# Kernel optimization log

Measured on AMD Instinct MI355X. Metric: run time of the kernel, lower is better.

Reference implementation:

```python
import jax, jax.numpy as jnp
import numpy as np
from jax import lax

GAMMA = 0.001  # init kwarg gamma
DN = ('NCHW', 'OIHW', 'NCHW')


def _maxpool2(x):
    # 2x2 max pool, stride 2, NCHW
    return lax.reduce_window(x, -jnp.inf, lax.max, (1, 1, 2, 2), (1, 1, 2, 2), 'VALID')


def _features(x, w1, b1, w2, b2):
    h = lax.conv_general_dilated(x, w1, (1, 1), 'SAME', dimension_numbers=DN)
    h = _maxpool2(jax.nn.relu(h + b1[None, :, None, None]))
    h = lax.conv_general_dilated(h, w2, (1, 1), 'SAME', dimension_numbers=DN)
    h = _maxpool2(jax.nn.relu(h + b2[None, :, None, None]))
    return h.reshape(h.shape[0], -1)  # [N, 16*7*7=784]


def setup_inputs() -> dict:
    key = jax.random.key(0)
    ks = jax.random.split(key, 7)
    x = jax.random.normal(ks[0], (4096, 1, 28, 28), dtype=jnp.float32)
    w1 = jax.random.normal(ks[1], (8, 1, 3, 3), dtype=jnp.float32) * 0.1
    b1 = jax.random.normal(ks[2], (8,), dtype=jnp.float32) * 0.1
    w2 = jax.random.normal(ks[3], (16, 8, 3, 3), dtype=jnp.float32) * 0.1
    b2 = jax.random.normal(ks[4], (16,), dtype=jnp.float32) * 0.1
    support = jax.random.uniform(ks[5], (8192, 784), dtype=jnp.float32)
    alpha = jax.random.normal(ks[6], (8192, 4), dtype=jnp.float32)
    return {'x': x, 'w1': w1, 'b1': b1, 'w2': w2, 'b2': b2,
            'support': support, 'alpha': alpha}


def reference(x, w1, b1, w2, b2, support, alpha):
    feats = _features(x, w1, b1, w2, b2)                      # [N, 784]
    # Pairwise squared distances via expansion (replaces the N*M python loop)
    f2 = jnp.sum(feats * feats, axis=1, keepdims=True)        # [N, 1]
    s2 = jnp.sum(support * support, axis=1)[None, :]          # [1, M]
    d2 = f2 + s2 - 2.0 * (feats @ support.T)                  # [N, M]
    K = jnp.exp(-GAMMA * d2)                                  # RBF kernel matrix
    return K @ alpha                                          # [N, n_classes]
```

## Files before the change

kernel.cpp:

```cpp
#include <hip/hip_runtime.h>
#include <hip/hip_bf16.h>
#include <cstdint>

#define GAMMA 0.001f
#define TILE_BYTES 114688

typedef __attribute__((ext_vector_type(4))) float f32x4;
typedef __attribute__((ext_vector_type(8))) int v8i;
typedef __attribute__((ext_vector_type(8))) short bh8;
typedef unsigned char u8;

__device__ inline unsigned pack4_fp8(float4 f) {
  unsigned p = __builtin_amdgcn_cvt_pk_fp8_f32(f.x, f.y, 0, false);
  p = __builtin_amdgcn_cvt_pk_fp8_f32(f.z, f.w, p, true);
  return p;
}

__device__ inline ushort bf16u(float v) {
  __hip_bfloat16 h = __float2bfloat16(v);
  return *(ushort*)&h;
}

__global__ __launch_bounds__(256, 4) void conv_prep_kernel(
    const float* __restrict__ x, const float* __restrict__ w1,
    const float* __restrict__ b1, const float* __restrict__ w2,
    const float* __restrict__ b2, const float* __restrict__ support,
    const float* __restrict__ alpha, u8* __restrict__ feats_t,
    u8* __restrict__ sup_t, float* __restrict__ beta,
    float* __restrict__ ef) {
  int tid = threadIdx.x;
  int bx = blockIdx.x;

  if (bx >= 2048) {
    int lane = tid & 63, wave = tid >> 6;
    int m = (bx - 2048) * 4 + wave;
    const float* row = support + (size_t)m * 784;
    int mt = m >> 7, mr = m & 127;
    u8* tb = sup_t + (size_t)mt * TILE_BYTES;
    float ss = 0.f;
    if (lane < 56) {
      uint4 w;
      if (lane < 49) {
        float4 f0 = ((const float4*)row)[lane * 4 + 0];
        float4 f1 = ((const float4*)row)[lane * 4 + 1];
        float4 f2 = ((const float4*)row)[lane * 4 + 2];
        float4 f3 = ((const float4*)row)[lane * 4 + 3];
        ss = f0.x * f0.x + f0.y * f0.y + f0.z * f0.z + f0.w * f0.w +
             f1.x * f1.x + f1.y * f1.y + f1.z * f1.z + f1.w * f1.w +
             f2.x * f2.x + f2.y * f2.y + f2.z * f2.z + f2.w * f2.w +
             f3.x * f3.x + f3.y * f3.y + f3.z * f3.z + f3.w * f3.w;
        w.x = pack4_fp8(f0); w.y = pack4_fp8(f1);
        w.z = pack4_fp8(f2); w.w = pack4_fp8(f3);
      } else {
        w.x = 0; w.y = 0; w.z = 0; w.w = 0;
      }
      int kk = lane >> 3, u = lane & 7, q = u >> 1, h = u & 1;
      int qs = q ^ ((mr >> 1) & 3);
      *(uint4*)(tb + kk * 16384 + h * 8192 + mr * 64 + qs * 16) = w;
    }
#pragma unroll
    for (int s = 1; s < 64; s <<= 1) ss += __shfl_xor(ss, s, 64);
    if (lane == 0) {
      float es = __expf(-GAMMA * ss);
      float4 a = ((const float4*)alpha)[m];
      float4 b;
      b.x = es * a.x; b.y = es * a.y; b.z = es * a.z; b.w = es * a.w;
      ((float4*)beta)[m] = b;
    }
    return;
  }

  __shared__ float xp[2][900];
  __shared__ alignas(16) ushort a1h[2][2048];
  __shared__ float w1s[72], b1s[8], b2s[16];
  __shared__ float w2s[1152];
  __shared__ alignas(8) ushort sc[2][16][212];
  __shared__ alignas(16) u8 fb[2][784];
  __shared__ float red[256];

  int lane = tid & 63, wave = tid >> 6;

  for (int t = tid; t < 1800; t += 256) ((float*)xp)[t] = 0.f;
  for (int t = tid; t < 1024; t += 256) ((uint4*)a1h)[t] = (uint4){0, 0, 0, 0};
  if (tid < 72) w1s[tid] = w1[tid];
  if (tid < 8) b1s[tid] = b1[tid];
  if (tid < 16) b2s[tid] = b2[tid];
  for (int t = tid; t < 1152; t += 256) w2s[t] = w2[t];
  __syncthreads();

  int oc = lane & 15, quad = lane >> 4;
  bh8 wf[3];
#pragma unroll
  for (int g = 0; g < 3; g++) {
    int tap = g * 4 + quad;
#pragma unroll
    for (int j = 0; j < 8; j++) {
      float v = (tap < 9) ? w2s[oc * 72 + j * 9 + tap] : 0.f;
      wf[g][j] = (short)bf16u(v);
    }
  }

  for (int t = tid; t < 392; t += 256) {
    int img = t >= 196, j = t - img * 196;
    float4 v = ((const float4*)(x + (size_t)(bx * 2 + img) * 784))[j];
    int r = j / 7, c = (j % 7) * 4;
    float* p = &xp[img][(r + 1) * 30 + (c + 1)];
    p[0] = v.x; p[1] = v.y; p[2] = v.z; p[3] = v.w;
  }
  __syncthreads();

  for (int idx = tid; idx < 3136; idx += 256) {
    int img = idx >= 1568;
    int rem = idx - img * 1568;
    int c = rem / 196, r2 = rem % 196;
    int ph = r2 / 14, pw = r2 % 14;
    const float* w = &w1s[c * 9];
    const float* xb = &xp[img][(2 * ph) * 30 + (2 * pw)];
    float t[4][4];
#pragma unroll
    for (int a = 0; a < 4; a++) {
      float2 u0 = *(const float2*)(xb + a * 30);
      float2 u1 = *(const float2*)(xb + a * 30 + 2);
      t[a][0] = u0.x; t[a][1] = u0.y; t[a][2] = u1.x; t[a][3] = u1.y;
    }
    float s00 = 0, s01 = 0, s10 = 0, s11 = 0;
#pragma unroll
    for (int dy = 0; dy < 3; dy++)
#pragma unroll
      for (int dx = 0; dx < 3; dx++) {
        float wv = w[dy * 3 + dx];
        s00 += t[dy][dx] * wv;     s01 += t[dy][dx + 1] * wv;
        s10 += t[dy + 1][dx] * wv; s11 += t[dy + 1][dx + 1] * wv;
      }
    float mx = fmaxf(fmaxf(s00, s01), fmaxf(s10, s11));
    float val = fmaxf(mx + b1s[c], 0.f);
    a1h[img][((ph + 1) * 16 + (pw + 1)) * 8 + c] = bf16u(val);
  }
  __syncthreads();

  {
    int img2 = wave >> 1, half = wave & 1;
    int Tstart = half * 7, Tcnt = half ? 6 : 7;
    const ushort* abase = a1h[img2];
    int mrow = lane & 15;
    for (int t = 0; t < Tcnt; ++t) {
      int T = Tstart + t;
      int p = T * 16 + mrow;
      int pc = p > 195 ? 195 : p;
      int y = pc / 14, xq = pc - y * 14;
      int cell = y * 16 + xq;
      f32x4 acc = (f32x4){0, 0, 0, 0};
#pragma unroll
      for (int g = 0; g < 3; g++) {
        int tap = g * 4 + quad;
        const ushort* ap;
        if (g == 2 && quad > 0) {
          ap = abase;
        } else {
          int dy = tap / 3, dx = tap - dy * 3;
          ap = abase + (cell + dy * 16 + dx) * 8;
        }
        bh8 af = *(const bh8*)ap;
        acc = __builtin_amdgcn_mfma_f32_16x16x32_bf16(af, wf[g], acc, 0, 0, 0);
      }
      int pos0 = T * 16 + quad * 4;
      ushort4 s4;
      s4.x = bf16u(acc.x); s4.y = bf16u(acc.y);
      s4.z = bf16u(acc.z); s4.w = bf16u(acc.w);
      *(ushort4*)(&sc[img2][oc][pos0]) = s4;
    }
  }
  __syncthreads();

  int img = tid >> 7, r = tid & 127;
  float fsq = 0.f;
  if (r < 112) {
    int o = r & 15, y7 = r >> 4;
    const ushort* srow = sc[img][o];
    float bo = b2s[o];
#pragma unroll
    for (int x7 = 0; x7 < 7; x7++) {
      int p = 28 * y7 + 2 * x7;
      unsigned u0 = *(const unsigned*)(&srow[p]);
      unsigned u1 = *(const unsigned*)(&srow[p + 14]);
      float a = __uint_as_float(u0 << 16);
      float b = __uint_as_float(u0 & 0xffff0000u);
      float c = __uint_as_float(u1 << 16);
      float d = __uint_as_float(u1 & 0xffff0000u);
      float mx = fmaxf(fmaxf(a, b), fmaxf(c, d));
      float val = fmaxf(mx + bo, 0.f);
      fb[img][o * 49 + y7 * 7 + x7] =
          (u8)(__builtin_amdgcn_cvt_pk_fp8_f32(val, 0.f, 0, false) & 0xff);
      fsq += val * val;
    }
  }
  red[tid] = fsq;
  __syncthreads();
  for (int s = 64; s > 0; s >>= 1) {
    if ((tid & 127) < s) red[tid] += red[tid + s];
    __syncthreads();
  }
  if ((tid & 127) == 0) ef[bx * 2 + img] = __expf(-GAMMA * red[tid]);

  if (tid < 112) {
    int im = tid >= 56, j = tid - im * 56;
    uint4 v;
    if (j < 49) v = ((const uint4*)fb[im])[j];
    else { v.x = 0; v.y = 0; v.z = 0; v.w = 0; }
    int n = bx * 2 + im;
    int nt = n >> 7, nr = n & 127;
    int kk = j >> 3, u = j & 7, q = u >> 1, h = u & 1;
    int qs = q ^ ((nr >> 1) & 3);
    *(uint4*)(feats_t + (size_t)nt * TILE_BYTES + kk * 16384 + h * 8192 +
              nr * 64 + qs * 16) = v;
  }
}

__global__ __launch_bounds__(256, 4) void rbf_gemm_kernel(
    const u8* __restrict__ feats_t, const u8* __restrict__ sup_t,
    const float* __restrict__ beta, float* __restrict__ partial) {
  int tid = threadIdx.x;
  int wave = tid >> 6, lane = tid & 63;
  int bx = blockIdx.x;
  int chunk = bx & 63, nb = bx >> 6;
  int wn = wave >> 1, wm = wave & 1;
  int col = lane & 15, quad = lane >> 4;
  int slot = quad ^ ((col >> 1) & 3);

  const u8* abase = feats_t + (size_t)nb * TILE_BYTES +
                    (wn * 64 + col) * 64 + slot * 16;
  const u8* bbase = sup_t + (size_t)chunk * TILE_BYTES +
                    (wm * 64 + col) * 64 + slot * 16;

  f32x4 acc[4][4];
#pragma unroll
  for (int i = 0; i < 4; i++)
#pragma unroll
    for (int j = 0; j < 4; j++) acc[i][j] = (f32x4){0, 0, 0, 0};

#define LDFRAG(p)                                                      \
  ({                                                                   \
    int4 lo_ = *(const int4*)(p);                                      \
    int4 hi_ = *(const int4*)((p) + 8192);                             \
    (v8i){lo_.x, lo_.y, lo_.z, lo_.w, hi_.x, hi_.y, hi_.z, hi_.w};     \
  })
#define MFMA(a, b, c)                                                  \
  __builtin_amdgcn_mfma_scale_f32_16x16x128_f8f6f4(                    \
      (a), (b), (c), 0, 0, 0, 0x7f7f7f7f, 0, 0x7f7f7f7f)

#pragma unroll 1
  for (int kk = 0; kk < 7; ++kk) {
    const u8* ak = abase + kk * 16384;
    const u8* bk = bbase + kk * 16384;
    v8i bv0 = LDFRAG(bk);
    v8i bv1 = LDFRAG(bk + 1024);
    v8i bv2 = LDFRAG(bk + 2048);
    v8i bv3 = LDFRAG(bk + 3072);
    v8i a0 = LDFRAG(ak);
    v8i a1 = LDFRAG(ak + 1024);
    acc[0][0] = MFMA(a0, bv0, acc[0][0]);
    acc[0][1] = MFMA(a0, bv1, acc[0][1]);
    acc[0][2] = MFMA(a0, bv2, acc[0][2]);
    acc[0][3] = MFMA(a0, bv3, acc[0][3]);
    a0 = LDFRAG(ak + 2048);
    acc[1][0] = MFMA(a1, bv0, acc[1][0]);
    acc[1][1] = MFMA(a1, bv1, acc[1][1]);
    acc[1][2] = MFMA(a1, bv2, acc[1][2]);
    acc[1][3] = MFMA(a1, bv3, acc[1][3]);
    a1 = LDFRAG(ak + 3072);
    acc[2][0] = MFMA(a0, bv0, acc[2][0]);
    acc[2][1] = MFMA(a0, bv1, acc[2][1]);
    acc[2][2] = MFMA(a0, bv2, acc[2][2]);
    acc[2][3] = MFMA(a0, bv3, acc[2][3]);
    acc[3][0] = MFMA(a1, bv0, acc[3][0]);
    acc[3][1] = MFMA(a1, bv1, acc[3][1]);
    acc[3][2] = MFMA(a1, bv2, acc[3][2]);
    acc[3][3] = MFMA(a1, bv3, acc[3][3]);
  }
#undef LDFRAG
#undef MFMA

#pragma unroll
  for (int i = 0; i < 4; i++)
#pragma unroll
    for (int j = 0; j < 4; j++) {
      acc[i][j].x = __expf(2.f * GAMMA * acc[i][j].x);
      acc[i][j].y = __expf(2.f * GAMMA * acc[i][j].y);
      acc[i][j].z = __expf(2.f * GAMMA * acc[i][j].z);
      acc[i][j].w = __expf(2.f * GAMMA * acc[i][j].w);
    }
  int n0 = nb * 128, m0 = chunk * 128;
#pragma unroll
  for (int c = 0; c < 4; ++c) {
    float bl[4];
#pragma unroll
    for (int j = 0; j < 4; j++)
      bl[j] = beta[(m0 + wm * 64 + j * 16 + col) * 4 + c];
#pragma unroll
    for (int i = 0; i < 4; i++) {
      f32x4 s = acc[i][0] * bl[0] + acc[i][1] * bl[1] + acc[i][2] * bl[2] +
                acc[i][3] * bl[3];
#pragma unroll
      for (int st = 1; st < 16; st <<= 1) {
        s.x += __shfl_xor(s.x, st, 16);
        s.y += __shfl_xor(s.y, st, 16);
        s.z += __shfl_xor(s.z, st, 16);
        s.w += __shfl_xor(s.w, st, 16);
      }
      if (col == c) {
        int n = n0 + wn * 64 + i * 16 + quad * 4;
        float* pp = partial + (((size_t)chunk * 2 + wm) * 4096 + n) * 4 + c;
        pp[0] = s.x; pp[4] = s.y; pp[8] = s.z; pp[12] = s.w;
      }
    }
  }
}

__global__ __launch_bounds__(256) void reduce_kernel(
    const float* __restrict__ partial, const float* __restrict__ ef,
    float* __restrict__ out) {
  __shared__ float4 sred[16][16];
  int nl = threadIdx.x & 15, sg = threadIdx.x >> 4;
  int n = blockIdx.x * 16 + nl;
  const float4* p = (const float4*)partial;
  float sx = 0, sy = 0, sz = 0, sw = 0;
#pragma unroll
  for (int ch = sg * 8; ch < sg * 8 + 8; ch++) {
    float4 v = p[(size_t)ch * 4096 + n];
    sx += v.x; sy += v.y; sz += v.z; sw += v.w;
  }
  sred[sg][nl] = (float4){sx, sy, sz, sw};
  __syncthreads();
  for (int st = 8; st > 0; st >>= 1) {
    if (sg < st) {
      float4 a = sred[sg][nl], b = sred[sg + st][nl];
      sred[sg][nl] = (float4){a.x + b.x, a.y + b.y, a.z + b.z, a.w + b.w};
    }
    __syncthreads();
  }
  if (sg == 0) {
    float e = ef[n];
    float4 a = sred[0][nl];
    ((float4*)out)[n] = (float4){e * a.x, e * a.y, e * a.z, e * a.w};
  }
}

extern "C" void kernel_launch(void* const* d_in, const int* in_sizes, int n_in,
                              void* d_out, int out_size, void* d_ws,
                              size_t ws_size, hipStream_t stream) {
  const float* x = (const float*)d_in[0];
  const float* w1 = (const float*)d_in[1];
  const float* b1 = (const float*)d_in[2];
  const float* w2 = (const float*)d_in[3];
  const float* b2 = (const float*)d_in[4];
  const float* support = (const float*)d_in[5];
  const float* alpha = (const float*)d_in[6];
  float* out = (float*)d_out;

  u8* ws = (u8*)d_ws;
  u8* sup_t = ws;
  u8* feats_t = ws + 7340032;
  float* beta = (float*)(ws + 11010048);
  float* ef = (float*)(ws + 11141120);
  float* partial = (float*)(ws + 11157504);

  conv_prep_kernel<<<4096, 256, 0, stream>>>(x, w1, b1, w2, b2, support, alpha,
                                             feats_t, sup_t, beta, ef);
  rbf_gemm_kernel<<<2048, 256, 0, stream>>>(feats_t, sup_t, beta, partial);
  reduce_kernel<<<256, 256, 0, stream>>>(partial, ef, out);
}
```

Before: 160.3 us.

## Fuse three kernels into one persistent cooperative kernel with grid syncs

Replaces the three separate launches (conv+prep, RBF GEMM, reduce) with a single cooperative persistent kernel. It loops over the original block indices and separates the phases with grid-wide syncs. The goal is to remove launch gaps and inter-kernel drain between phases. The costs are a smaller grid that may reduce occupancy for the heavy phases, two grid barriers, and extra shared-memory pressure from the fused kernel. If the cooperative launch fails, the code falls back to the original three launches.

```diff
diff --git a/kernel.cpp b/kernel.cpp
--- a/kernel.cpp
+++ b/kernel.cpp
@@ -1,6 +1,9 @@
 #include <hip/hip_runtime.h>
 #include <hip/hip_bf16.h>
+#include <hip/hip_cooperative_groups.h>
 #include <cstdint>
+
+namespace cg = cooperative_groups;
 
 #define GAMMA 0.001f
 #define TILE_BYTES 114688
@@ -19,6 +22,334 @@
 __device__ inline ushort bf16u(float v) {
   __hip_bfloat16 h = __float2bfloat16(v);
   return *(ushort*)&h;
+}
+
+__global__ __launch_bounds__(256, 4) void fused_kernel(
+    const float* __restrict__ x, const float* __restrict__ w1,
+    const float* __restrict__ b1, const float* __restrict__ w2,
+    const float* __restrict__ b2, const float* __restrict__ support,
+    const float* __restrict__ alpha, u8* __restrict__ feats_t,
+    u8* __restrict__ sup_t, float* __restrict__ beta, float* __restrict__ ef,
+    float* __restrict__ partial, float* __restrict__ out) {
+  __shared__ alignas(16) float xp[2][900];
+  __shared__ alignas(16) ushort a1h[2][2048];
+  __shared__ float w1s[72], b1s[8], b2s[16];
+  __shared__ float w2s[1152];
+  __shared__ alignas(8) ushort sc[2][16][212];
+  __shared__ alignas(16) u8 fb[2][784];
+  __shared__ float red[256];
+
+  int tid = threadIdx.x;
+  int lane = tid & 63, wave = tid >> 6;
+
+  for (int cbx = blockIdx.x; cbx < 2048; cbx += gridDim.x) {
+    __syncthreads();
+
+    for (int t = tid; t < 1800; t += 256) ((float*)xp)[t] = 0.f;
+    for (int t = tid; t < 1024; t += 256)
+      ((uint4*)a1h)[t] = (uint4){0, 0, 0, 0};
+    if (tid < 72) w1s[tid] = w1[tid];
+    if (tid < 8) b1s[tid] = b1[tid];
+    if (tid < 16) b2s[tid] = b2[tid];
+    for (int t = tid; t < 1152; t += 256) w2s[t] = w2[t];
+    __syncthreads();
+
+    int oc = lane & 15, quad = lane >> 4;
+    bh8 wf[3];
+#pragma unroll
+    for (int g = 0; g < 3; g++) {
+      int tap = g * 4 + quad;
+#pragma unroll
+      for (int j = 0; j < 8; j++) {
+        float v = (tap < 9) ? w2s[oc * 72 + j * 9 + tap] : 0.f;
+        wf[g][j] = (short)bf16u(v);
+      }
+    }
+
+    for (int t = tid; t < 392; t += 256) {
+      int img = t >= 196, j = t - img * 196;
+      float4 v = ((const float4*)(x + (size_t)(cbx * 2 + img) * 784))[j];
+      int r = j / 7, c = (j % 7) * 4;
+      float* p = &xp[img][(r + 1) * 30 + (c + 1)];
+      p[0] = v.x; p[1] = v.y; p[2] = v.z; p[3] = v.w;
+    }
+    __syncthreads();
+
+    for (int idx = tid; idx < 3136; idx += 256) {
+      int img = idx >= 1568;
+      int rem = idx - img * 1568;
+      int c = rem / 196, r2 = rem % 196;
+      int ph = r2 / 14, pw = r2 % 14;
+      const float* w = &w1s[c * 9];
+      const float* xb = &xp[img][(2 * ph) * 30 + (2 * pw)];
+      float t[4][4];
+#pragma unroll
+      for (int a = 0; a < 4; a++) {
+        float2 u0 = *(const float2*)(xb + a * 30);
+        float2 u1 = *(const float2*)(xb + a * 30 + 2);
+        t[a][0] = u0.x; t[a][1] = u0.y; t[a][2] = u1.x; t[a][3] = u1.y;
+      }
+      float s00 = 0, s01 = 0, s10 = 0, s11 = 0;
+#pragma unroll
+      for (int dy = 0; dy < 3; dy++)
+#pragma unroll
+        for (int dx = 0; dx < 3; dx++) {
+          float wv = w[dy * 3 + dx];
+          s00 += t[dy][dx] * wv;     s01 += t[dy][dx + 1] * wv;
+          s10 += t[dy + 1][dx] * wv; s11 += t[dy + 1][dx + 1] * wv;
+        }
+      float mx = fmaxf(fmaxf(s00, s01), fmaxf(s10, s11));
+      float val = fmaxf(mx + b1s[c], 0.f);
+      a1h[img][((ph + 1) * 16 + (pw + 1)) * 8 + c] = bf16u(val);
+    }
+    __syncthreads();
+
+    {
+      int img2 = wave >> 1, half = wave & 1;
+      int Tstart = half * 7, Tcnt = half ? 6 : 7;
+      const ushort* abase = a1h[img2];
+      int mrow = lane & 15;
+      for (int t = 0; t < Tcnt; ++t) {
+        int T = Tstart + t;
+        int p = T * 16 + mrow;
+        int pc = p > 195 ? 195 : p;
+        int y = pc / 14, xq = pc - y * 14;
+        int cell = y * 16 + xq;
+        f32x4 acc = (f32x4){0, 0, 0, 0};
+#pragma unroll
+        for (int g = 0; g < 3; g++) {
+          int tap = g * 4 + quad;
+          const ushort* ap;
+          if (g == 2 && quad > 0) {
+            ap = abase;
+          } else {
+            int dy = tap / 3, dx = tap - dy * 3;
+            ap = abase + (cell + dy * 16 + dx) * 8;
+          }
+          bh8 af = *(const bh8*)ap;
+          acc =
+              __builtin_amdgcn_mfma_f32_16x16x32_bf16(af, wf[g], acc, 0, 0, 0);
+        }
+        int pos0 = T * 16 + quad * 4;
+        ushort4 s4;
+        s4.x = bf16u(acc.x); s4.y = bf16u(acc.y);
+        s4.z = bf16u(acc.z); s4.w = bf16u(acc.w);
+        *(ushort4*)(&sc[img2][oc][pos0]) = s4;
+      }
+    }
+    __syncthreads();
+
+    int img = tid >> 7, r = tid & 127;
+    float fsq = 0.f;
+    if (r < 112) {
+      int o = r & 15, y7 = r >> 4;
+      const ushort* srow = sc[img][o];
+      float bo = b2s[o];
+#pragma unroll
+      for (int x7 = 0; x7 < 7; x7++) {
+        int p = 28 * y7 + 2 * x7;
+        unsigned u0 = *(const unsigned*)(&srow[p]);
+        unsigned u1 = *(const unsigned*)(&srow[p + 14]);
+        float a = __uint_as_float(u0 << 16);
+        float b = __uint_as_float(u0 & 0xffff0000u);
+        float c = __uint_as_float(u1 << 16);
+        float d = __uint_as_float(u1 & 0xffff0000u);
+        float mx = fmaxf(fmaxf(a, b), fmaxf(c, d));
+        float val = fmaxf(mx + bo, 0.f);
+        fb[img][o * 49 + y7 * 7 + x7] =
+            (u8)(__builtin_amdgcn_cvt_pk_fp8_f32(val, 0.f, 0, false) & 0xff);
+        fsq += val * val;
+      }
+    }
+    red[tid] = fsq;
+    __syncthreads();
+    for (int s = 64; s > 0; s >>= 1) {
+      if ((tid & 127) < s) red[tid] += red[tid + s];
+      __syncthreads();
+    }
+    if ((tid & 127) == 0) ef[cbx * 2 + img] = __expf(-GAMMA * red[tid]);
+
+    if (tid < 112) {
+      int im = tid >= 56, j = tid - im * 56;
+      uint4 v;
+      if (j < 49) v = ((const uint4*)fb[im])[j];
+      else { v.x = 0; v.y = 0; v.z = 0; v.w = 0; }
+      int n = cbx * 2 + im;
+      int nt = n >> 7, nr = n & 127;
+      int kk = j >> 3, u = j & 7, q = u >> 1, h = u & 1;
+      int qs = q ^ ((nr >> 1) & 3);
+      *(uint4*)(feats_t + (size_t)nt * TILE_BYTES + kk * 16384 + h * 8192 +
+                nr * 64 + qs * 16) = v;
+    }
+  }
+
+  for (int sb = blockIdx.x; sb < 2048; sb += gridDim.x) {
+    int m = sb * 4 + wave;
+    const float* row = support + (size_t)m * 784;
+    int mt = m >> 7, mr = m & 127;
+    u8* tb = sup_t + (size_t)mt * TILE_BYTES;
+    float ss = 0.f;
+    if (lane < 56) {
+      uint4 w;
+      if (lane < 49) {
+        float4 f0 = ((const float4*)row)[lane * 4 + 0];
+        float4 f1 = ((const float4*)row)[lane * 4 + 1];
+        float4 f2 = ((const float4*)row)[lane * 4 + 2];
+        float4 f3 = ((const float4*)row)[lane * 4 + 3];
+        ss = f0.x * f0.x + f0.y * f0.y + f0.z * f0.z + f0.w * f0.w +
+             f1.x * f1.x + f1.y * f1.y + f1.z * f1.z + f1.w * f1.w +
+             f2.x * f2.x + f2.y * f2.y + f2.z * f2.z + f2.w * f2.w +
+             f3.x * f3.x + f3.y * f3.y + f3.z * f3.z + f3.w * f3.w;
+        w.x = pack4_fp8(f0); w.y = pack4_fp8(f1);
+        w.z = pack4_fp8(f2); w.w = pack4_fp8(f3);
+      } else {
+        w.x = 0; w.y = 0; w.z = 0; w.w = 0;
+      }
+      int kk = lane >> 3, u = lane & 7, q = u >> 1, h = u & 1;
+      int qs = q ^ ((mr >> 1) & 3);
+      *(uint4*)(tb + kk * 16384 + h * 8192 + mr * 64 + qs * 16) = w;
+    }
+#pragma unroll
+    for (int s = 1; s < 64; s <<= 1) ss += __shfl_xor(ss, s, 64);
+    if (lane == 0) {
+      float es = __expf(-GAMMA * ss);
+      float4 a = ((const float4*)alpha)[m];
+      float4 b;
+      b.x = es * a.x; b.y = es * a.y; b.z = es * a.z; b.w = es * a.w;
+      ((float4*)beta)[m] = b;
+    }
+  }
+
+  __threadfence();
+  cg::this_grid().sync();
+
+#define LDFRAG(p)                                                      \
+  ({                                                                   \
+    int4 lo_ = *(const int4*)(p);                                      \
+    int4 hi_ = *(const int4*)((p) + 8192);                             \
+    (v8i){lo_.x, lo_.y, lo_.z, lo_.w, hi_.x, hi_.y, hi_.z, hi_.w};     \
+  })
+#define MFMA(a, b, c)                                                  \
+  __builtin_amdgcn_mfma_scale_f32_16x16x128_f8f6f4(                    \
+      (a), (b), (c), 0, 0, 0, 0x7f7f7f7f, 0, 0x7f7f7f7f)
+
+  for (int gbx = blockIdx.x; gbx < 2048; gbx += gridDim.x) {
+    int chunk = gbx & 63, nb = gbx >> 6;
+    int wn = wave >> 1, wm = wave & 1;
+    int col = lane & 15, quad = lane >> 4;
+    int slot = quad ^ ((col >> 1) & 3);
+
+    const u8* abase = feats_t + (size_t)nb * TILE_BYTES +
+                      (wn * 64 + col) * 64 + slot * 16;
+    const u8* bbase = sup_t + (size_t)chunk * TILE_BYTES +
+                      (wm * 64 + col) * 64 + slot * 16;
+
+    f32x4 acc[4][4];
+#pragma unroll
+    for (int i = 0; i < 4; i++)
+#pragma unroll
+      for (int j = 0; j < 4; j++) acc[i][j] = (f32x4){0, 0, 0, 0};
+
+#pragma unroll 1
+    for (int kk = 0; kk < 7; ++kk) {
+      const u8* ak = abase + kk * 16384;
+      const u8* bk = bbase + kk * 16384;
+      v8i bv0 = LDFRAG(bk);
+      v8i bv1 = LDFRAG(bk + 1024);
+      v8i bv2 = LDFRAG(bk + 2048);
+      v8i bv3 = LDFRAG(bk + 3072);
+      v8i a0 = LDFRAG(ak);
+      v8i a1 = LDFRAG(ak + 1024);
+      acc[0][0] = MFMA(a0, bv0, acc[0][0]);
+      acc[0][1] = MFMA(a0, bv1, acc[0][1]);
+      acc[0][2] = MFMA(a0, bv2, acc[0][2]);
+      acc[0][3] = MFMA(a0, bv3, acc[0][3]);
+      a0 = LDFRAG(ak + 2048);
+      acc[1][0] = MFMA(a1, bv0, acc[1][0]);
+      acc[1][1] = MFMA(a1, bv1, acc[1][1]);
+      acc[1][2] = MFMA(a1, bv2, acc[1][2]);
+      acc[1][3] = MFMA(a1, bv3, acc[1][3]);
+      a1 = LDFRAG(ak + 3072);
+      acc[2][0] = MFMA(a0, bv0, acc[2][0]);
+      acc[2][1] = MFMA(a0, bv1, acc[2][1]);
+      acc[2][2] = MFMA(a0, bv2, acc[2][2]);
+      acc[2][3] = MFMA(a0, bv3, acc[2][3]);
+      acc[3][0] = MFMA(a1, bv0, acc[3][0]);
+      acc[3][1] = MFMA(a1, bv1, acc[3][1]);
+      acc[3][2] = MFMA(a1, bv2, acc[3][2]);
+      acc[3][3] = MFMA(a1, bv3, acc[3][3]);
+    }
+
+#pragma unroll
+    for (int i = 0; i < 4; i++)
+#pragma unroll
+      for (int j = 0; j < 4; j++) {
+        acc[i][j].x = __expf(2.f * GAMMA * acc[i][j].x);
+        acc[i][j].y = __expf(2.f * GAMMA * acc[i][j].y);
+        acc[i][j].z = __expf(2.f * GAMMA * acc[i][j].z);
+        acc[i][j].w = __expf(2.f * GAMMA * acc[i][j].w);
+      }
+    int n0 = nb * 128, m0 = chunk * 128;
+#pragma unroll
+    for (int c = 0; c < 4; ++c) {
+      float bl[4];
+#pragma unroll
+      for (int j = 0; j < 4; j++)
+        bl[j] = beta[(m0 + wm * 64 + j * 16 + col) * 4 + c];
+#pragma unroll
+      for (int i = 0; i < 4; i++) {
+        f32x4 s = acc[i][0] * bl[0] + acc[i][1] * bl[1] + acc[i][2] * bl[2] +
+                  acc[i][3] * bl[3];
+#pragma unroll
+        for (int st = 1; st < 16; st <<= 1) {
+          s.x += __shfl_xor(s.x, st, 16);
+          s.y += __shfl_xor(s.y, st, 16);
+          s.z += __shfl_xor(s.z, st, 16);
+          s.w += __shfl_xor(s.w, st, 16);
+        }
+        if (col == c) {
+          int n = n0 + wn * 64 + i * 16 + quad * 4;
+          float* pp = partial + (((size_t)chunk * 2 + wm) * 4096 + n) * 4 + c;
+          pp[0] = s.x; pp[4] = s.y; pp[8] = s.z; pp[12] = s.w;
+        }
+      }
+    }
+  }
+#undef LDFRAG
+#undef MFMA
+
+  __threadfence();
+  cg::this_grid().sync();
+
+  {
+    float4(*sred)[16] = (float4(*)[16])xp;
+    int nl = tid & 15, sg = tid >> 4;
+    for (int rb = blockIdx.x; rb < 256; rb += gridDim.x) {
+      int n = rb * 16 + nl;
+      const float4* p = (const float4*)partial;
+      float sx = 0, sy = 0, sz = 0, sw = 0;
+#pragma unroll
+      for (int ch = sg * 8; ch < sg * 8 + 8; ch++) {
+        float4 v = p[(size_t)ch * 4096 + n];
+        sx += v.x; sy += v.y; sz += v.z; sw += v.w;
+      }
+      sred[sg][nl] = (float4){sx, sy, sz, sw};
+      __syncthreads();
+      for (int st = 8; st > 0; st >>= 1) {
+        if (sg < st) {
+          float4 a = sred[sg][nl], b = sred[sg + st][nl];
+          sred[sg][nl] = (float4){a.x + b.x, a.y + b.y, a.z + b.z, a.w + b.w};
+        }
+        __syncthreads();
+      }
+      if (sg == 0) {
+        float e = ef[n];
+        float4 a = sred[0][nl];
+        ((float4*)out)[n] = (float4){e * a.x, e * a.y, e * a.z, e * a.w};
+      }
+      __syncthreads();
+    }
+  }
 }
 
 __global__ __launch_bounds__(256, 4) void conv_prep_kernel(
@@ -364,8 +695,32 @@
   float* ef = (float*)(ws + 11141120);
   float* partial = (float*)(ws + 11157504);
 
-  conv_prep_kernel<<<4096, 256, 0, stream>>>(x, w1, b1, w2, b2, support, alpha,
-                                             feats_t, sup_t, beta, ef);
-  rbf_gemm_kernel<<<2048, 256, 0, stream>>>(feats_t, sup_t, beta, partial);
-  reduce_kernel<<<256, 256, 0, stream>>>(partial, ef, out);
+  static int coop_grid = 0;
+  if (coop_grid == 0) {
+    int per_cu = 0;
+    if (hipOccupancyMaxActiveBlocksPerMultiprocessor(
+            &per_cu, (const void*)fused_kernel, 256, 0) != hipSuccess ||
+        per_cu <= 0)
+      per_cu = 2;
+    if (per_cu > 4) per_cu = 4;
+    coop_grid = per_cu * 256;
+    if (coop_grid > 1024) coop_grid = 1024;
+    if (coop_grid < 256) coop_grid = 256;
+  }
+
+  void* kargs[] = {(void*)&x,       (void*)&w1,      (void*)&b1,
+                   (void*)&w2,      (void*)&b2,      (void*)&support,
+                   (void*)&alpha,   (void*)&feats_t, (void*)&sup_t,
+                   (void*)&beta,    (void*)&ef,      (void*)&partial,
+                   (void*)&out};
+  hipError_t err = hipLaunchCooperativeKernel(
+      (const void*)fused_kernel, dim3(coop_grid), dim3(256), kargs, 0, stream);
+  if (err != hipSuccess) {
+    (void)hipGetLastError();
+    conv_prep_kernel<<<4096, 256, 0, stream>>>(x, w1, b1, w2, b2, support,
+                                               alpha, feats_t, sup_t, beta,
+                                               ef);
+    rbf_gemm_kernel<<<2048, 256, 0, stream>>>(feats_t, sup_t, beta, partial);
+    reduce_kernel<<<256, 256, 0, stream>>>(partial, ef, out);
+  }
 }
```

After: 452.9 us. 2.82x slower.

## Fuse final partial reduction into GEMM via last-block atomic ticket

Applied to the files above, without the earlier changes.

Removes the separate reduce kernel launch. Each GEMM block increments a per-row-tile counter after writing its partials, and the last of the 64 chunk blocks for that tile sums all partials, scales by ef, and writes the output. Counters are zeroed in the prep kernel. This saves a launch and its tail gap, at the cost of atomics, fences and a serialized reduction inside one tail block per tile.

```diff
diff --git a/kernel.cpp b/kernel.cpp
--- a/kernel.cpp
+++ b/kernel.cpp
@@ -26,10 +26,12 @@
     const float* __restrict__ b1, const float* __restrict__ w2,
     const float* __restrict__ b2, const float* __restrict__ support,
     const float* __restrict__ alpha, u8* __restrict__ feats_t,
-    u8* __restrict__ sup_t, float* __restrict__ beta,
-    float* __restrict__ ef) {
+    u8* __restrict__ sup_t, float* __restrict__ beta, float* __restrict__ ef,
+    unsigned* __restrict__ counters) {
   int tid = threadIdx.x;
   int bx = blockIdx.x;
+
+  if (bx == 0 && tid < 32) counters[tid] = 0;
 
   if (bx >= 2048) {
     int lane = tid & 63, wave = tid >> 6;
@@ -218,7 +220,11 @@
 
 __global__ __launch_bounds__(256, 4) void rbf_gemm_kernel(
     const u8* __restrict__ feats_t, const u8* __restrict__ sup_t,
-    const float* __restrict__ beta, float* __restrict__ partial) {
+    const float* __restrict__ beta, float* __restrict__ partial,
+    const float* __restrict__ ef, float* __restrict__ out,
+    unsigned* __restrict__ counters) {
+  __shared__ float4 sred[128];
+  __shared__ unsigned sticket;
   int tid = threadIdx.x;
   int wave = tid >> 6, lane = tid & 63;
   int bx = blockIdx.x;
@@ -314,34 +320,32 @@
       }
     }
   }
-}
-
-__global__ __launch_bounds__(256) void reduce_kernel(
-    const float* __restrict__ partial, const float* __restrict__ ef,
-    float* __restrict__ out) {
-  __shared__ float4 sred[16][16];
-  int nl = threadIdx.x & 15, sg = threadIdx.x >> 4;
-  int n = blockIdx.x * 16 + nl;
-  const float4* p = (const float4*)partial;
-  float sx = 0, sy = 0, sz = 0, sw = 0;
-#pragma unroll
-  for (int ch = sg * 8; ch < sg * 8 + 8; ch++) {
-    float4 v = p[(size_t)ch * 4096 + n];
-    sx += v.x; sy += v.y; sz += v.z; sw += v.w;
-  }
-  sred[sg][nl] = (float4){sx, sy, sz, sw};
-  __syncthreads();
-  for (int st = 8; st > 0; st >>= 1) {
-    if (sg < st) {
-      float4 a = sred[sg][nl], b = sred[sg + st][nl];
-      sred[sg][nl] = (float4){a.x + b.x, a.y + b.y, a.z + b.z, a.w + b.w};
-    }
+
+  __syncthreads();
+  if (tid == 0) {
+    __threadfence();
+    sticket = atomicAdd(&counters[nb], 1u);
+  }
+  __syncthreads();
+  if (sticket == 63u) {
+    __threadfence();
+    int nl = tid & 127, sg = tid >> 7;
+    int n = n0 + nl;
+    const float4* p4 = (const float4*)partial;
+    float sx = 0.f, sy = 0.f, sz = 0.f, sw = 0.f;
+    for (int ch = sg * 64; ch < sg * 64 + 64; ch++) {
+      float4 v = p4[(size_t)ch * 4096 + n];
+      sx += v.x; sy += v.y; sz += v.z; sw += v.w;
+    }
+    if (sg == 1) sred[nl] = (float4){sx, sy, sz, sw};
     __syncthreads();
-  }
-  if (sg == 0) {
-    float e = ef[n];
-    float4 a = sred[0][nl];
-    ((float4*)out)[n] = (float4){e * a.x, e * a.y, e * a.z, e * a.w};
+    if (sg == 0) {
+      float4 b = sred[nl];
+      float e = ef[n];
+      ((float4*)out)[n] =
+          (float4){e * (sx + b.x), e * (sy + b.y), e * (sz + b.z),
+                   e * (sw + b.w)};
+    }
   }
 }
 
@@ -363,9 +367,11 @@
   float* beta = (float*)(ws + 11010048);
   float* ef = (float*)(ws + 11141120);
   float* partial = (float*)(ws + 11157504);
+  unsigned* counters = (unsigned*)(ws + 19546112);
 
   conv_prep_kernel<<<4096, 256, 0, stream>>>(x, w1, b1, w2, b2, support, alpha,
-                                             feats_t, sup_t, beta, ef);
-  rbf_gemm_kernel<<<2048, 256, 0, stream>>>(feats_t, sup_t, beta, partial);
-  reduce_kernel<<<256, 256, 0, stream>>>(partial, ef, out);
-}
+                                             feats_t, sup_t, beta, ef,
+                                             counters);
+  rbf_gemm_kernel<<<2048, 256, 0, stream>>>(feats_t, sup_t, beta, partial, ef,
+                                            out, counters);
+}
```

New measurement: 267.4 us. 1.67x slower.
